# Performance work log

Measured on AMD Instinct MI355X. Metric: run time of the kernel, lower is better.

Reference implementation:

```python
import jax, jax.numpy as jnp
import numpy as np

B, N, IN_DIM, HID, OUT, E = 2, 50000, 64, 256, 128, 500000

def setup_inputs() -> dict:
    key = jax.random.key(0)
    ks = jax.random.split(key, 8)
    s = lambda fan_in: 1.0 / np.sqrt(fan_in)
    x = jax.random.normal(ks[0], (B, N, IN_DIM), dtype=jnp.float32)
    edges = jax.random.randint(ks[1], (E, 2), 0, N, dtype=jnp.int64)
    return {
        "x": x,
        "edges": edges,
        "ew1": jax.random.normal(ks[2], (2 * IN_DIM, HID), dtype=jnp.float32) * s(2 * IN_DIM),
        "eb1": jnp.zeros((HID,), jnp.float32),
        "ew2": jax.random.normal(ks[3], (HID, OUT), dtype=jnp.float32) * s(HID),
        "eb2": jnp.zeros((OUT,), jnp.float32),
        "nw1": jax.random.normal(ks[4], (IN_DIM, HID), dtype=jnp.float32) * s(IN_DIM),
        "nb1": jnp.zeros((HID,), jnp.float32),
        "nw2": jax.random.normal(ks[5], (HID, OUT), dtype=jnp.float32) * s(HID),
        "nb2": jnp.zeros((OUT,), jnp.float32),
        "dw": jax.random.normal(ks[6], (OUT, IN_DIM), dtype=jnp.float32) * s(OUT),
        "db": jnp.zeros((IN_DIM,), jnp.float32),
    }

def _mlp(z, w1, b1, w2, b2):
    return jax.nn.relu(z @ w1 + b1) @ w2 + b2

def reference(x, edges, ew1, eb1, ew2, eb2, nw1, nb1, nw2, nb2, dw, db):
    u, v = edges[:, 0], edges[:, 1]
    # node embedding: [B, N, OUT]
    h = _mlp(x, nw1, nb1, nw2, nb2)
    # per-edge MLP on concatenated endpoint features: [B, E, OUT]
    edge_input = jnp.concatenate([x[:, u], x[:, v]], axis=-1)  # [B, E, 2*IN]
    edge_emb = _mlp(edge_input, ew1, eb1, ew2, eb2)
    # scatter-add edge message to both endpoints
    messages = jnp.zeros_like(h).at[:, u].add(edge_emb).at[:, v].add(edge_emb)
    h = h + messages
    recon = h @ dw + db  # [B, N, IN]
    return recon
```

## Files before the change

### kernel.cpp

```cpp
#include <hip/hip_runtime.h>
#include <hip/hip_bf16.h>

#define BB   2
#define NN   50000
#define BN   100000
#define NE   500000
#define NSB  196

#define EPITCH 136
#define XPITCH 72
#define HPITCH 264
#define RPITCH 72

using u16 = unsigned short;
using u32 = unsigned int;
typedef __attribute__((ext_vector_type(8))) short short8;
typedef __attribute__((ext_vector_type(4))) short short4v;
typedef __attribute__((ext_vector_type(4))) float f32x4;

__device__ __forceinline__ u16 f2bf(float f) {
    union { float f; u32 u; } w; w.f = f;
    return (u16)((w.u + 0x7fffu + ((w.u >> 16) & 1u)) >> 16);
}

#if defined(__has_builtin)
#if __has_builtin(__builtin_amdgcn_cvt_pk_bf16_f32)
#define HAVE_CVTPK 1
#endif
#endif

__device__ __forceinline__ u32 pack_bf(float lo, float hi) {
#ifdef HAVE_CVTPK
    auto r = __builtin_amdgcn_cvt_pk_bf16_f32(lo, hi);
    u32 out; __builtin_memcpy(&out, &r, sizeof(out));
    return out;
#else
    return ((u32)f2bf(hi) << 16) | (u32)f2bf(lo);
#endif
}

__global__ __launch_bounds__(256) void csr_zero(int* __restrict__ cursor) {
    int i = blockIdx.x * 256 + threadIdx.x;
    if (i < NN) cursor[i] = 0;
}

__global__ __launch_bounds__(256) void csr_hist(const int* __restrict__ edges,
                                                int* __restrict__ cursor) {
    int e = blockIdx.x * 256 + threadIdx.x;
    if (e < NE) {
        atomicAdd(&cursor[edges[2*e]], 1);
        atomicAdd(&cursor[edges[2*e+1]], 1);
    }
}

__global__ __launch_bounds__(256) void scan_pass1(const int* __restrict__ cursor,
                                                  int* __restrict__ bsum) {
    __shared__ int s[256];
    const int t = threadIdx.x;
    int i = blockIdx.x * 256 + t;
    s[t] = (i < NN) ? cursor[i] : 0;
    __syncthreads();
    for (int d = 128; d > 0; d >>= 1) {
        if (t < d) s[t] += s[t + d];
        __syncthreads();
    }
    if (t == 0) bsum[blockIdx.x] = s[0];
}

__global__ __launch_bounds__(256) void scan_pass2(const int* __restrict__ bsum,
                                                  int* __restrict__ boff) {
    __shared__ int s[256];
    const int t = threadIdx.x;
    s[t] = (t < NSB) ? bsum[t] : 0;
    __syncthreads();
    for (int d = 1; d < 256; d <<= 1) {
        int v = (t >= d) ? s[t - d] : 0;
        __syncthreads();
        s[t] += v;
        __syncthreads();
    }
    if (t <= NSB) boff[t] = (t == 0) ? 0 : s[t - 1];
}

__global__ __launch_bounds__(256) void scan_pass3(int* __restrict__ cursor,
                                                  const int* __restrict__ boff,
                                                  int* __restrict__ off) {
    __shared__ int s[256];
    const int t = threadIdx.x;
    int i = blockIdx.x * 256 + t;
    int v = (i < NN) ? cursor[i] : 0;
    s[t] = v;
    __syncthreads();
    for (int d = 1; d < 256; d <<= 1) {
        int p = (t >= d) ? s[t - d] : 0;
        __syncthreads();
        s[t] += p;
        __syncthreads();
    }
    int excl = boff[blockIdx.x] + s[t] - v;
    if (i < NN) { off[i] = excl; cursor[i] = excl; }
    if (i == NN - 1) off[NN] = excl + v;
}

__global__ __launch_bounds__(256) void csr_fill(const int* __restrict__ edges,
                                                int* __restrict__ cursor,
                                                int* __restrict__ pos) {
    int e = blockIdx.x * 256 + threadIdx.x;
    if (e < NE) {
        pos[2*e]     = atomicAdd(&cursor[edges[2*e]], 1);
        pos[2*e + 1] = atomicAdd(&cursor[edges[2*e+1]], 1);
    }
}

__global__ __launch_bounds__(256) void swizzle_w1(
    const float* __restrict__ ew1, const float* __restrict__ nw1,
    u16* __restrict__ frag)
{
    int idx = blockIdx.x * 256 + threadIdx.x;
    if (idx >= 49152) return;
    const float* src; int KB, local;
    if (idx < 32768) { local = idx;         src = ew1; KB = 4; }
    else             { local = idx - 32768; src = nw1; KB = 2; }
    int j = local & 7, l = (local >> 3) & 63, rest = local >> 9;
    int kblk = rest % KB, ntile = rest / KB;
    int n = ntile * 16 + (l & 15);
    int k = kblk * 32 + ((l >> 4) << 3) + j;
    frag[idx] = f2bf(src[k * 256 + n]);
}

__global__ __launch_bounds__(256) void fuse_w2(
    const float* __restrict__ ew2, const float* __restrict__ nw2,
    const float* __restrict__ dw, u16* __restrict__ frag)
{
    int idx = blockIdx.x * 256 + threadIdx.x;
    if (idx >= 32768) return;
    const float* src = (idx < 16384) ? ew2 : nw2;
    int local = idx & 16383;
    int j = local & 7, l = (local >> 3) & 63, rest = local >> 9;
    int kblk = rest & 7, ntile = rest >> 3;
    int n = ntile * 16 + (l & 15);
    int k = kblk * 32 + ((l >> 4) << 3) + j;
    float s = 0.f;
    for (int jj = 0; jj < 128; ++jj) s = fmaf(src[k * 128 + jj], dw[jj * 64 + n], s);
    frag[49152 + idx] = f2bf(s);
}

__global__ __launch_bounds__(128) void fuse_bias(
    const float* __restrict__ eb2, const float* __restrict__ nb2,
    const float* __restrict__ dw, const float* __restrict__ db,
    float* __restrict__ bias2)
{
    int t = threadIdx.x;
    int d = t & 63;
    const float* bsrc = (t >= 64) ? nb2 : eb2;
    float s = 0.f;
    #pragma unroll 4
    for (int j = 0; j < 128; ++j) s = fmaf(bsrc[j], dw[j * 64 + d], s);
    if (t >= 64) bias2[64 + d] = s + db[d];
    else         bias2[d] = s;
}

__global__ __launch_bounds__(256) void node_mlp_kernel(
    const float* __restrict__ x, const float* __restrict__ nb1,
    const float* __restrict__ bias2, const u16* __restrict__ frag,
    u16* __restrict__ xbf, float* __restrict__ out)
{
    __shared__ u16 xs[64 * XPITCH];
    __shared__ u16 hid[64 * HPITCH];
    const int t = threadIdx.x;
    const int wave = t >> 6, l = t & 63, lane15 = l & 15, quad = l >> 4;
    const int r0 = blockIdx.x * 64;
    const int valid = min(64, BN - r0);

    #pragma unroll
    for (int it = 0; it < 4; ++it) {
        int i = t + it * 256;
        int m = i >> 4, c4 = i & 15;
        int row = min(r0 + m, BN - 1);
        float4 g = ((const float4*)x)[(size_t)row * 16 + c4];
        uint2 q = make_uint2(pack_bf(g.x, g.y), pack_bf(g.z, g.w));
        *(uint2*)(xs + m * XPITCH + c4 * 4) = q;
        *(uint2*)(xbf + (size_t)row * 64 + c4 * 4) = q;
    }
    __syncthreads();

    {
        f32x4 acc[4][4];
        #pragma unroll
        for (int i = 0; i < 4; ++i)
            #pragma unroll
            for (int mt = 0; mt < 4; ++mt) acc[i][mt] = f32x4{0.f,0.f,0.f,0.f};
        const u16* w1 = frag + 32768;
        #pragma unroll
        for (int kblk = 0; kblk < 2; ++kblk) {
            short8 bf[4], af[4];
            #pragma unroll
            for (int mt = 0; mt < 4; ++mt)
                bf[mt] = *(const short8*)(xs + (mt*16 + lane15) * XPITCH + kblk*32 + quad*8);
            #pragma unroll
            for (int i = 0; i < 4; ++i)
                af[i] = *(const short8*)(w1 + (((wave*4 + i)*2 + kblk)*64 + l) * 8);
            #pragma unroll
            for (int i = 0; i < 4; ++i)
                #pragma unroll
                for (int mt = 0; mt < 4; ++mt)
                    acc[i][mt] = __builtin_amdgcn_mfma_f32_16x16x32_bf16(af[i], bf[mt], acc[i][mt], 0, 0, 0);
        }
        #pragma unroll
        for (int i = 0; i < 4; ++i) {
            int n0 = (wave*4 + i)*16 + quad*4;
            float4 bv = *(const float4*)(nb1 + n0);
            #pragma unroll
            for (int mt = 0; mt < 4; ++mt) {
                int m = mt*16 + lane15;
                uint2 q = make_uint2(
                    pack_bf(fmaxf(acc[i][mt][0] + bv.x, 0.f), fmaxf(acc[i][mt][1] + bv.y, 0.f)),
                    pack_bf(fmaxf(acc[i][mt][2] + bv.z, 0.f), fmaxf(acc[i][mt][3] + bv.w, 0.f)));
                *(uint2*)(hid + m * HPITCH + n0) = q;
            }
        }
    }
    __syncthreads();

    {
        f32x4 acc[4];
        #pragma unroll
        for (int mt = 0; mt < 4; ++mt) acc[mt] = f32x4{0.f,0.f,0.f,0.f};
        const u16* w2 = frag + 65536;
        #pragma unroll
        for (int kblk = 0; kblk < 8; ++kblk) {
            short8 bf[4], af;
            #pragma unroll
            for (int mt = 0; mt < 4; ++mt)
                bf[mt] = *(const short8*)(hid + (mt*16 + lane15) * HPITCH + kblk*32 + quad*8);
            af = *(const short8*)(w2 + ((wave*8 + kblk)*64 + l) * 8);
            #pragma unroll
            for (int mt = 0; mt < 4; ++mt)
                acc[mt] = __builtin_amdgcn_mfma_f32_16x16x32_bf16(af, bf[mt], acc[mt], 0, 0, 0);
        }
        int n0 = wave*16 + quad*4;
        float4 bv = *(const float4*)(bias2 + 64 + n0);
        #pragma unroll
        for (int mt = 0; mt < 4; ++mt) {
            int m = mt*16 + lane15;
            if (m < valid) {
                float4 o;
                o.x = acc[mt][0] + bv.x; o.y = acc[mt][1] + bv.y;
                o.z = acc[mt][2] + bv.z; o.w = acc[mt][3] + bv.w;
                *(float4*)(out + (size_t)(r0 + m) * 64 + n0) = o;
            }
        }
    }
}

__global__ __launch_bounds__(256) void edge_emb_kernel(
    const u16* __restrict__ xbf, const int* __restrict__ edges,
    const float* __restrict__ eb1, const float* __restrict__ bias2,
    const u16* __restrict__ frag, const int* __restrict__ pos,
    u16* __restrict__ perm, int b)
{
    __shared__ u16 ein[64 * EPITCH];
    __shared__ u16 hid[64 * HPITCH];
    __shared__ int us[64], vs[64], ps[64], qs[64];
    const int t = threadIdx.x;
    const int wave = t >> 6, l = t & 63, lane15 = l & 15, quad = l >> 4;
    const int e0 = blockIdx.x * 64;
    const int valid = min(64, NE - e0);

    if (t < 64) {
        int e = min(e0 + t, NE - 1);
        us[t] = edges[2 * e];
        vs[t] = edges[2 * e + 1];
        ps[t] = pos[2 * e];
        qs[t] = pos[2 * e + 1];
    }
    __syncthreads();

    #pragma unroll
    for (int it = 0; it < 4; ++it) {
        int i = t + it * 256;
        int m = i >> 4, c = i & 15;
        int half = c >> 3, c8 = c & 7;
        int node = half ? vs[m] : us[m];
        uint4 q = ((const uint4*)xbf)[(size_t)(b * NN + node) * 8 + c8];
        *(uint4*)(ein + m * EPITCH + half * 64 + c8 * 8) = q;
    }
    __syncthreads();

    {
        f32x4 acc[4][4];
        #pragma unroll
        for (int i = 0; i < 4; ++i)
            #pragma unroll
            for (int mt = 0; mt < 4; ++mt) acc[i][mt] = f32x4{0.f,0.f,0.f,0.f};
        const u16* w1 = frag;
        #pragma unroll
        for (int kblk = 0; kblk < 4; ++kblk) {
            short8 bf[4], af[4];
            #pragma unroll
            for (int mt = 0; mt < 4; ++mt)
                bf[mt] = *(const short8*)(ein + (mt*16 + lane15) * EPITCH + kblk*32 + quad*8);
            #pragma unroll
            for (int i = 0; i < 4; ++i)
                af[i] = *(const short8*)(w1 + (((wave*4 + i)*4 + kblk)*64 + l) * 8);
            #pragma unroll
            for (int i = 0; i < 4; ++i)
                #pragma unroll
                for (int mt = 0; mt < 4; ++mt)
                    acc[i][mt] = __builtin_amdgcn_mfma_f32_16x16x32_bf16(af[i], bf[mt], acc[i][mt], 0, 0, 0);
        }
        #pragma unroll
        for (int i = 0; i < 4; ++i) {
            int n0 = (wave*4 + i)*16 + quad*4;
            float4 bv = *(const float4*)(eb1 + n0);
            #pragma unroll
            for (int mt = 0; mt < 4; ++mt) {
                int m = mt*16 + lane15;
                uint2 q = make_uint2(
                    pack_bf(fmaxf(acc[i][mt][0] + bv.x, 0.f), fmaxf(acc[i][mt][1] + bv.y, 0.f)),
                    pack_bf(fmaxf(acc[i][mt][2] + bv.z, 0.f), fmaxf(acc[i][mt][3] + bv.w, 0.f)));
                *(uint2*)(hid + m * HPITCH + n0) = q;
            }
        }
    }
    __syncthreads();

    {
        f32x4 acc[4];
        #pragma unroll
        for (int mt = 0; mt < 4; ++mt) acc[mt] = f32x4{0.f,0.f,0.f,0.f};
        const u16* w2 = frag + 49152;
        #pragma unroll
        for (int kblk = 0; kblk < 8; ++kblk) {
            short8 bf[4], af;
            #pragma unroll
            for (int mt = 0; mt < 4; ++mt)
                bf[mt] = *(const short8*)(hid + (mt*16 + lane15) * HPITCH + kblk*32 + quad*8);
            af = *(const short8*)(w2 + ((wave*8 + kblk)*64 + l) * 8);
            #pragma unroll
            for (int mt = 0; mt < 4; ++mt)
                acc[mt] = __builtin_amdgcn_mfma_f32_16x16x32_bf16(af, bf[mt], acc[mt], 0, 0, 0);
        }
        int n0 = wave*16 + quad*4;
        float4 bv = *(const float4*)(bias2 + n0);
        #pragma unroll
        for (int mt = 0; mt < 4; ++mt) {
            int m = mt*16 + lane15;
            uint2 q = make_uint2(
                pack_bf(acc[mt][0] + bv.x, acc[mt][1] + bv.y),
                pack_bf(acc[mt][2] + bv.z, acc[mt][3] + bv.w));
            *(uint2*)(ein + m * RPITCH + n0) = q;
        }
    }
    __syncthreads();

    #pragma unroll
    for (int it = 0; it < 4; ++it) {
        int i = t + it * 256;
        int dest = i >> 3, c8 = i & 7;
        int m = dest >> 1;
        if (m < valid) {
            int p = (dest & 1) ? qs[m] : ps[m];
            ((uint4*)(perm + (size_t)p * 64))[c8] = *(const uint4*)(ein + m * RPITCH + c8 * 8);
        }
    }
}

__global__ __launch_bounds__(256) void gather_kernel(
    const u32* __restrict__ perm32, const int* __restrict__ off,
    float* __restrict__ out, int b)
{
    const int t = threadIdx.x, wave = t >> 6, l = t & 63;
    const int n = blockIdx.x * 4 + wave;
    const int base = off[n], cnt = off[n + 1] - base;
    if (cnt == 0) return;
    const int slot = l >> 4, c8h = l & 15;
    float a0 = 0.f, a1 = 0.f, a2 = 0.f, a3 = 0.f;
    for (int j0 = 0; j0 < cnt; j0 += 8) {
        int jA = j0 + slot, jB = j0 + 4 + slot;
        const u32* rpA = perm32 + (size_t)(base + min(jA, cnt - 1)) * 32 + 2 * c8h;
        const u32* rpB = perm32 + (size_t)(base + min(jB, cnt - 1)) * 32 + 2 * c8h;
        u32 wA0 = rpA[0], wA1 = rpA[1];
        u32 wB0 = rpB[0], wB1 = rpB[1];
        union { u32 u; float f; } x0, x1, x2, x3;
        if (jA < cnt) {
            x0.u = wA0 << 16; x1.u = wA0 & 0xffff0000u;
            x2.u = wA1 << 16; x3.u = wA1 & 0xffff0000u;
            a0 += x0.f; a1 += x1.f; a2 += x2.f; a3 += x3.f;
        }
        if (jB < cnt) {
            x0.u = wB0 << 16; x1.u = wB0 & 0xffff0000u;
            x2.u = wB1 << 16; x3.u = wB1 & 0xffff0000u;
            a0 += x0.f; a1 += x1.f; a2 += x2.f; a3 += x3.f;
        }
    }
    a0 += __shfl_xor(a0, 16); a1 += __shfl_xor(a1, 16);
    a2 += __shfl_xor(a2, 16); a3 += __shfl_xor(a3, 16);
    a0 += __shfl_xor(a0, 32); a1 += __shfl_xor(a1, 32);
    a2 += __shfl_xor(a2, 32); a3 += __shfl_xor(a3, 32);
    if (l < 16) {
        float4* p = (float4*)(out + (size_t)(b * NN + n) * 64 + 4 * l);
        float4 h = *p;
        h.x += a0; h.y += a1; h.z += a2; h.w += a3;
        *p = h;
    }
}

extern "C" void kernel_launch(void* const* d_in, const int* in_sizes, int n_in,
                              void* d_out, int out_size, void* d_ws, size_t ws_size,
                              hipStream_t stream) {
    const float* x     = (const float*)d_in[0];
    const int*   edges = (const int*)d_in[1];
    const float* ew1   = (const float*)d_in[2];
    const float* eb1   = (const float*)d_in[3];
    const float* ew2   = (const float*)d_in[4];
    const float* eb2   = (const float*)d_in[5];
    const float* nw1   = (const float*)d_in[6];
    const float* nb1   = (const float*)d_in[7];
    const float* nw2   = (const float*)d_in[8];
    const float* nb2   = (const float*)d_in[9];
    const float* dw    = (const float*)d_in[10];
    const float* db    = (const float*)d_in[11];
    float* out = (float*)d_out;

    char* w = (char*)d_ws;
    size_t o = 0;
    auto take = [&](size_t bytes) { char* p = w + o; o = (o + bytes + 511) & ~(size_t)511; return p; };
    u16*   frag   = (u16*)  take(81920 * 2);
    float* bias2  = (float*)take(128 * 4);
    int*   cursor = (int*)  take((size_t)NN * 4);
    int*   off    = (int*)  take((size_t)(NN + 1) * 4);
    int*   bsum   = (int*)  take((size_t)(NSB + 1) * 4);
    int*   boff   = (int*)  take((size_t)(NSB + 1) * 4);
    int*   pos    = (int*)  take((size_t)2 * NE * 4);
    u16*   xbf    = (u16*)  take((size_t)BN * 64 * 2);
    u16*   perm   = (u16*)  take((size_t)2 * NE * 64 * 2);

    csr_zero<<<NSB, 256, 0, stream>>>(cursor);
    csr_hist<<<(NE + 255) / 256, 256, 0, stream>>>(edges, cursor);
    scan_pass1<<<NSB, 256, 0, stream>>>(cursor, bsum);
    scan_pass2<<<1, 256, 0, stream>>>(bsum, boff);
    scan_pass3<<<NSB, 256, 0, stream>>>(cursor, boff, off);
    csr_fill<<<(NE + 255) / 256, 256, 0, stream>>>(edges, cursor, pos);

    swizzle_w1<<<192, 256, 0, stream>>>(ew1, nw1, frag);
    fuse_w2<<<128, 256, 0, stream>>>(ew2, nw2, dw, frag);
    fuse_bias<<<1, 128, 0, stream>>>(eb2, nb2, dw, db, bias2);

    node_mlp_kernel<<<(BN + 63) / 64, 256, 0, stream>>>(x, nb1, bias2, frag, xbf, out);

    for (int b = 0; b < BB; ++b) {
        edge_emb_kernel<<<(NE + 63) / 64, 256, 0, stream>>>(xbf, edges, eb1, bias2, frag, pos, perm, b);
        gather_kernel<<<NN / 4, 256, 0, stream>>>((const u32*)perm, off, out, b);
    }
}
```

Measured before the change: 452.9 us.

## Swizzle LDS tiles, merge weight-prep kernels, batch both graphs in one launch

Replaces the padded LDS pitches with XOR-swizzled unpadded layouts for the input, hidden and result tiles, so MFMA fragment loads avoid bank conflicts while using less shared memory. Merges the three weight-preparation kernels into a single launch. When the workspace can hold two permutation buffers, the edge and gather kernels run both batches in one 2D grid, cutting launches and giving each launch more parallelism. The trade-off is a doubled permutation buffer and an extra code path that depends on workspace size.

```diff
diff --git a/kernel.cpp b/kernel.cpp
--- a/kernel.cpp
+++ b/kernel.cpp
@@ -7,15 +7,9 @@
 #define NE   500000
 #define NSB  196
 
-#define EPITCH 136
-#define XPITCH 72
-#define HPITCH 264
-#define RPITCH 72
-
 using u16 = unsigned short;
 using u32 = unsigned int;
 typedef __attribute__((ext_vector_type(8))) short short8;
-typedef __attribute__((ext_vector_type(4))) short short4v;
 typedef __attribute__((ext_vector_type(4))) float f32x4;
 
 __device__ __forceinline__ u16 f2bf(float f) {
@@ -112,52 +106,44 @@
     }
 }
 
-__global__ __launch_bounds__(256) void swizzle_w1(
+__global__ __launch_bounds__(256) void weight_prep(
     const float* __restrict__ ew1, const float* __restrict__ nw1,
-    u16* __restrict__ frag)
+    const float* __restrict__ ew2, const float* __restrict__ nw2,
+    const float* __restrict__ dw,  const float* __restrict__ db,
+    const float* __restrict__ eb2, const float* __restrict__ nb2,
+    u16* __restrict__ frag, float* __restrict__ bias2)
 {
-    int idx = blockIdx.x * 256 + threadIdx.x;
-    if (idx >= 49152) return;
-    const float* src; int KB, local;
-    if (idx < 32768) { local = idx;         src = ew1; KB = 4; }
-    else             { local = idx - 32768; src = nw1; KB = 2; }
-    int j = local & 7, l = (local >> 3) & 63, rest = local >> 9;
-    int kblk = rest % KB, ntile = rest / KB;
-    int n = ntile * 16 + (l & 15);
-    int k = kblk * 32 + ((l >> 4) << 3) + j;
-    frag[idx] = f2bf(src[k * 256 + n]);
-}
-
-__global__ __launch_bounds__(256) void fuse_w2(
-    const float* __restrict__ ew2, const float* __restrict__ nw2,
-    const float* __restrict__ dw, u16* __restrict__ frag)
-{
-    int idx = blockIdx.x * 256 + threadIdx.x;
-    if (idx >= 32768) return;
-    const float* src = (idx < 16384) ? ew2 : nw2;
-    int local = idx & 16383;
-    int j = local & 7, l = (local >> 3) & 63, rest = local >> 9;
-    int kblk = rest & 7, ntile = rest >> 3;
-    int n = ntile * 16 + (l & 15);
-    int k = kblk * 32 + ((l >> 4) << 3) + j;
-    float s = 0.f;
-    for (int jj = 0; jj < 128; ++jj) s = fmaf(src[k * 128 + jj], dw[jj * 64 + n], s);
-    frag[49152 + idx] = f2bf(s);
-}
-
-__global__ __launch_bounds__(128) void fuse_bias(
-    const float* __restrict__ eb2, const float* __restrict__ nb2,
-    const float* __restrict__ dw, const float* __restrict__ db,
-    float* __restrict__ bias2)
-{
-    int t = threadIdx.x;
-    int d = t & 63;
-    const float* bsrc = (t >= 64) ? nb2 : eb2;
-    float s = 0.f;
-    #pragma unroll 4
-    for (int j = 0; j < 128; ++j) s = fmaf(bsrc[j], dw[j * 64 + d], s);
-    if (t >= 64) bias2[64 + d] = s + db[d];
-    else         bias2[d] = s;
+    int blk = blockIdx.x, t = threadIdx.x;
+    if (blk < 192) {
+        int idx = blk * 256 + t;
+        const float* src; int KB, local;
+        if (idx < 32768) { local = idx;         src = ew1; KB = 4; }
+        else             { local = idx - 32768; src = nw1; KB = 2; }
+        int j = local & 7, l = (local >> 3) & 63, rest = local >> 9;
+        int kblk = rest % KB, ntile = rest / KB;
+        int n = ntile * 16 + (l & 15);
+        int k = kblk * 32 + ((l >> 4) << 3) + j;
+        frag[idx] = f2bf(src[k * 256 + n]);
+    } else if (blk < 320) {
+        int idx = (blk - 192) * 256 + t;
+        const float* src = (idx < 16384) ? ew2 : nw2;
+        int local = idx & 16383;
+        int j = local & 7, l = (local >> 3) & 63, rest = local >> 9;
+        int kblk = rest & 7, ntile = rest >> 3;
+        int n = ntile * 16 + (l & 15);
+        int k = kblk * 32 + ((l >> 4) << 3) + j;
+        float s = 0.f;
+        for (int jj = 0; jj < 128; ++jj) s = fmaf(src[k * 128 + jj], dw[jj * 64 + n], s);
+        frag[49152 + idx] = f2bf(s);
+    } else if (t < 128) {
+        int d = t & 63;
+        const float* bsrc = (t >= 64) ? nb2 : eb2;
+        float s = 0.f;
+        #pragma unroll 4
+        for (int j = 0; j < 128; ++j) s = fmaf(bsrc[j], dw[j * 64 + d], s);
+        if (t >= 64) bias2[64 + d] = s + db[d];
+        else         bias2[d] = s;
+    }
 }
 
 __global__ __launch_bounds__(256) void node_mlp_kernel(
@@ -165,8 +151,8 @@
     const float* __restrict__ bias2, const u16* __restrict__ frag,
     u16* __restrict__ xbf, float* __restrict__ out)
 {
-    __shared__ u16 xs[64 * XPITCH];
-    __shared__ u16 hid[64 * HPITCH];
+    __shared__ u16 xs[64 * 64];
+    __shared__ u16 hid[64 * 256];
     const int t = threadIdx.x;
     const int wave = t >> 6, l = t & 63, lane15 = l & 15, quad = l >> 4;
     const int r0 = blockIdx.x * 64;
@@ -179,7 +165,8 @@
         int row = min(r0 + m, BN - 1);
         float4 g = ((const float4*)x)[(size_t)row * 16 + c4];
         uint2 q = make_uint2(pack_bf(g.x, g.y), pack_bf(g.z, g.w));
-        *(uint2*)(xs + m * XPITCH + c4 * 4) = q;
+        int chunk = c4 >> 1;
+        *(uint2*)(xs + m * 64 + ((chunk ^ (m & 7)) << 3) + (c4 & 1) * 4) = q;
         *(uint2*)(xbf + (size_t)row * 64 + c4 * 4) = q;
     }
     __syncthreads();
@@ -194,9 +181,12 @@
         #pragma unroll
         for (int kblk = 0; kblk < 2; ++kblk) {
             short8 bf[4], af[4];
-            #pragma unroll
-            for (int mt = 0; mt < 4; ++mt)
-                bf[mt] = *(const short8*)(xs + (mt*16 + lane15) * XPITCH + kblk*32 + quad*8);
+            int chunk = kblk * 4 + quad;
+            #pragma unroll
+            for (int mt = 0; mt < 4; ++mt) {
+                int row = mt*16 + lane15;
+                bf[mt] = *(const short8*)(xs + row * 64 + ((chunk ^ (row & 7)) << 3));
+            }
             #pragma unroll
             for (int i = 0; i < 4; ++i)
                 af[i] = *(const short8*)(w1 + (((wave*4 + i)*2 + kblk)*64 + l) * 8);
@@ -209,14 +199,15 @@
         #pragma unroll
         for (int i = 0; i < 4; ++i) {
             int n0 = (wave*4 + i)*16 + quad*4;
+            int chunk = (wave*4 + i)*2 + (quad >> 1);
             float4 bv = *(const float4*)(nb1 + n0);
             #pragma unroll
             for (int mt = 0; mt < 4; ++mt) {
-                int m = mt*16 + lane15;
+                int row = mt*16 + lane15;
                 uint2 q = make_uint2(
                     pack_bf(fmaxf(acc[i][mt][0] + bv.x, 0.f), fmaxf(acc[i][mt][1] + bv.y, 0.f)),
                     pack_bf(fmaxf(acc[i][mt][2] + bv.z, 0.f), fmaxf(acc[i][mt][3] + bv.w, 0.f)));
-                *(uint2*)(hid + m * HPITCH + n0) = q;
+                *(uint2*)(hid + row * 256 + ((chunk ^ (row & 15)) << 3) + (quad & 1) * 4) = q;
             }
         }
     }
@@ -230,9 +221,12 @@
         #pragma unroll
         for (int kblk = 0; kblk < 8; ++kblk) {
             short8 bf[4], af;
-            #pragma unroll
-            for (int mt = 0; mt < 4; ++mt)
-                bf[mt] = *(const short8*)(hid + (mt*16 + lane15) * HPITCH + kblk*32 + quad*8);
+            int chunk = kblk * 4 + quad;
+            #pragma unroll
+            for (int mt = 0; mt < 4; ++mt) {
+                int row = mt*16 + lane15;
+                bf[mt] = *(const short8*)(hid + row * 256 + ((chunk ^ (row & 15)) << 3));
+            }
             af = *(const short8*)(w2 + ((wave*8 + kblk)*64 + l) * 8);
             #pragma unroll
             for (int mt = 0; mt < 4; ++mt)
@@ -257,13 +251,15 @@
     const u16* __restrict__ xbf, const int* __restrict__ edges,
     const float* __restrict__ eb1, const float* __restrict__ bias2,
     const u16* __restrict__ frag, const int* __restrict__ pos,
-    u16* __restrict__ perm, int b)
+    u16* __restrict__ perm, int b_base, size_t pstride16)
 {
-    __shared__ u16 ein[64 * EPITCH];
-    __shared__ u16 hid[64 * HPITCH];
+    __shared__ u16 ein[64 * 128];
+    __shared__ u16 hid[64 * 256];
     __shared__ int us[64], vs[64], ps[64], qs[64];
     const int t = threadIdx.x;
     const int wave = t >> 6, l = t & 63, lane15 = l & 15, quad = l >> 4;
+    const int b = b_base + blockIdx.y;
+    u16* permb = perm + pstride16 * blockIdx.y;
     const int e0 = blockIdx.x * 64;
     const int valid = min(64, NE - e0);
 
@@ -283,7 +279,7 @@
         int half = c >> 3, c8 = c & 7;
         int node = half ? vs[m] : us[m];
         uint4 q = ((const uint4*)xbf)[(size_t)(b * NN + node) * 8 + c8];
-        *(uint4*)(ein + m * EPITCH + half * 64 + c8 * 8) = q;
+        *(uint4*)(ein + m * 128 + ((c ^ (m & 15)) << 3)) = q;
     }
     __syncthreads();
 
@@ -297,9 +293,12 @@
         #pragma unroll
         for (int kblk = 0; kblk < 4; ++kblk) {
             short8 bf[4], af[4];
-            #pragma unroll
-            for (int mt = 0; mt < 4; ++mt)
-                bf[mt] = *(const short8*)(ein + (mt*16 + lane15) * EPITCH + kblk*32 + quad*8);
+            int chunk = kblk * 4 + quad;
+            #pragma unroll
+            for (int mt = 0; mt < 4; ++mt) {
+                int row = mt*16 + lane15;
+                bf[mt] = *(const short8*)(ein + row * 128 + ((chunk ^ (row & 15)) << 3));
+            }
             #pragma unroll
             for (int i = 0; i < 4; ++i)
                 af[i] = *(const short8*)(w1 + (((wave*4 + i)*4 + kblk)*64 + l) * 8);
@@ -312,14 +311,15 @@
         #pragma unroll
         for (int i = 0; i < 4; ++i) {
             int n0 = (wave*4 + i)*16 + quad*4;
+            int chunk = (wave*4 + i)*2 + (quad >> 1);
             float4 bv = *(const float4*)(eb1 + n0);
             #pragma unroll
             for (int mt = 0; mt < 4; ++mt) {
-                int m = mt*16 + lane15;
+                int row = mt*16 + lane15;
                 uint2 q = make_uint2(
                     pack_bf(fmaxf(acc[i][mt][0] + bv.x, 0.f), fmaxf(acc[i][mt][1] + bv.y, 0.f)),
                     pack_bf(fmaxf(acc[i][mt][2] + bv.z, 0.f), fmaxf(acc[i][mt][3] + bv.w, 0.f)));
-                *(uint2*)(hid + m * HPITCH + n0) = q;
+                *(uint2*)(hid + row * 256 + ((chunk ^ (row & 15)) << 3) + (quad & 1) * 4) = q;
             }
         }
     }
@@ -333,15 +333,19 @@
         #pragma unroll
         for (int kblk = 0; kblk < 8; ++kblk) {
             short8 bf[4], af;
-            #pragma unroll
-            for (int mt = 0; mt < 4; ++mt)
-                bf[mt] = *(const short8*)(hid + (mt*16 + lane15) * HPITCH + kblk*32 + quad*8);
+            int chunk = kblk * 4 + quad;
+            #pragma unroll
+            for (int mt = 0; mt < 4; ++mt) {
+                int row = mt*16 + lane15;
+                bf[mt] = *(const short8*)(hid + row * 256 + ((chunk ^ (row & 15)) << 3));
+            }
             af = *(const short8*)(w2 + ((wave*8 + kblk)*64 + l) * 8);
             #pragma unroll
             for (int mt = 0; mt < 4; ++mt)
                 acc[mt] = __builtin_amdgcn_mfma_f32_16x16x32_bf16(af, bf[mt], acc[mt], 0, 0, 0);
         }
         int n0 = wave*16 + quad*4;
+        int chunk = wave*2 + (quad >> 1);
         float4 bv = *(const float4*)(bias2 + n0);
         #pragma unroll
         for (int mt = 0; mt < 4; ++mt) {
@@ -349,7 +353,7 @@
             uint2 q = make_uint2(
                 pack_bf(acc[mt][0] + bv.x, acc[mt][1] + bv.y),
                 pack_bf(acc[mt][2] + bv.z, acc[mt][3] + bv.w));
-            *(uint2*)(ein + m * RPITCH + n0) = q;
+            *(uint2*)(ein + m * 64 + ((chunk ^ (m & 7)) << 3) + (quad & 1) * 4) = q;
         }
     }
     __syncthreads();
@@ -361,16 +365,19 @@
         int m = dest >> 1;
         if (m < valid) {
             int p = (dest & 1) ? qs[m] : ps[m];
-            ((uint4*)(perm + (size_t)p * 64))[c8] = *(const uint4*)(ein + m * RPITCH + c8 * 8);
+            ((uint4*)(permb + (size_t)p * 64))[c8] =
+                *(const uint4*)(ein + m * 64 + ((c8 ^ (m & 7)) << 3));
         }
     }
 }
 
 __global__ __launch_bounds__(256) void gather_kernel(
     const u32* __restrict__ perm32, const int* __restrict__ off,
-    float* __restrict__ out, int b)
+    float* __restrict__ out, int b_base, size_t pstride16)
 {
     const int t = threadIdx.x, wave = t >> 6, l = t & 63;
+    const int b = b_base + blockIdx.y;
+    const u32* permb = perm32 + (pstride16 >> 1) * blockIdx.y;
     const int n = blockIdx.x * 4 + wave;
     const int base = off[n], cnt = off[n + 1] - base;
     if (cnt == 0) return;
@@ -378,8 +385,8 @@
     float a0 = 0.f, a1 = 0.f, a2 = 0.f, a3 = 0.f;
     for (int j0 = 0; j0 < cnt; j0 += 8) {
         int jA = j0 + slot, jB = j0 + 4 + slot;
-        const u32* rpA = perm32 + (size_t)(base + min(jA, cnt - 1)) * 32 + 2 * c8h;
-        const u32* rpB = perm32 + (size_t)(base + min(jB, cnt - 1)) * 32 + 2 * c8h;
+        const u32* rpA = permb + (size_t)(base + min(jA, cnt - 1)) * 32 + 2 * c8h;
+        const u32* rpB = permb + (size_t)(base + min(jB, cnt - 1)) * 32 + 2 * c8h;
         u32 wA0 = rpA[0], wA1 = rpA[1];
         u32 wB0 = rpB[0], wB1 = rpB[1];
         union { u32 u; float f; } x0, x1, x2, x3;
@@ -434,7 +441,10 @@
     int*   boff   = (int*)  take((size_t)(NSB + 1) * 4);
     int*   pos    = (int*)  take((size_t)2 * NE * 4);
     u16*   xbf    = (u16*)  take((size_t)BN * 64 * 2);
-    u16*   perm   = (u16*)  take((size_t)2 * NE * 64 * 2);
+    const size_t permElems = (size_t)2 * NE * 64;
+    u16*   perm   = (u16*)  take(permElems * 2);
+    bool dual = (o + permElems * 2) <= ws_size;
+    if (dual) take(permElems * 2);
 
     csr_zero<<<NSB, 256, 0, stream>>>(cursor);
     csr_hist<<<(NE + 255) / 256, 256, 0, stream>>>(edges, cursor);
@@ -443,14 +453,21 @@
     scan_pass3<<<NSB, 256, 0, stream>>>(cursor, boff, off);
     csr_fill<<<(NE + 255) / 256, 256, 0, stream>>>(edges, cursor, pos);
 
-    swizzle_w1<<<192, 256, 0, stream>>>(ew1, nw1, frag);
-    fuse_w2<<<128, 256, 0, stream>>>(ew2, nw2, dw, frag);
-    fuse_bias<<<1, 128, 0, stream>>>(eb2, nb2, dw, db, bias2);
+    weight_prep<<<321, 256, 0, stream>>>(ew1, nw1, ew2, nw2, dw, db, eb2, nb2, frag, bias2);
 
     node_mlp_kernel<<<(BN + 63) / 64, 256, 0, stream>>>(x, nb1, bias2, frag, xbf, out);
 
-    for (int b = 0; b < BB; ++b) {
-        edge_emb_kernel<<<(NE + 63) / 64, 256, 0, stream>>>(xbf, edges, eb1, bias2, frag, pos, perm, b);
-        gather_kernel<<<NN / 4, 256, 0, stream>>>((const u32*)perm, off, out, b);
-    }
-}
+    if (dual) {
+        edge_emb_kernel<<<dim3((NE + 63) / 64, BB), 256, 0, stream>>>(
+            xbf, edges, eb1, bias2, frag, pos, perm, 0, permElems);
+        gather_kernel<<<dim3(NN / 4, BB), 256, 0, stream>>>(
+            (const u32*)perm, off, out, 0, permElems);
+    } else {
+        for (int b = 0; b < BB; ++b) {
+            edge_emb_kernel<<<dim3((NE + 63) / 64, 1), 256, 0, stream>>>(
+                xbf, edges, eb1, bias2, frag, pos, perm, b, 0);
+            gather_kernel<<<dim3(NN / 4, 1), 256, 0, stream>>>(
+                (const u32*)perm, off, out, b, 0);
+        }
+    }
+}
```

New measurement: 445.3 us. Within noise of the previous version (-1.7%).
